# Kernel tuning notes

Hardware: AMD Instinct MI355X
Metric: run time of the kernel (lower is better)

## Reference

```python
import jax, jax.numpy as jnp
import numpy as np
import math

DIM = 512
HEADS = 8
DHEAD = DIM // HEADS            # 64
NB_FEATURES = int(DHEAD * math.log(DHEAD))  # 266
B, N = 2, 2048
CHUNK = 128                     # chunk size for the causal scan
EPS = 1e-4


def gaussian_orthogonal_random_matrix(nb_rows, nb_cols, rng):
    # blocks of orthogonal rows (Q^T of QR of a gaussian), scaled by chi-distributed norms
    blocks = []
    n_full = nb_rows // nb_cols
    for _ in range(n_full):
        q, _ = np.linalg.qr(rng.standard_normal((nb_cols, nb_cols)))
        blocks.append(q.T)
    rem = nb_rows - n_full * nb_cols
    if rem > 0:
        q, _ = np.linalg.qr(rng.standard_normal((nb_cols, nb_cols)))
        blocks.append(q.T[:rem])
    mat = np.concatenate(blocks, axis=0)
    multiplier = np.linalg.norm(rng.standard_normal((nb_rows, nb_cols)), axis=1)
    return (multiplier[:, None] * mat).astype(np.float32)


def setup_inputs() -> dict:
    key = jax.random.key(0)
    k1, k2, k3 = jax.random.split(key, 3)
    rng = np.random.default_rng(0)
    x = jax.random.normal(k1, (B, N, DIM), dtype=jnp.float32)
    w_qkv = jax.random.normal(k2, (DIM, 3 * DIM), dtype=jnp.float32) / math.sqrt(DIM)
    w_out = jax.random.normal(k3, (DIM, DIM), dtype=jnp.float32) / math.sqrt(DIM)
    b_out = jnp.zeros((DIM,), dtype=jnp.float32)
    proj = jnp.asarray(gaussian_orthogonal_random_matrix(NB_FEATURES, DHEAD, rng))
    return {"x": x, "w_qkv": w_qkv, "w_out": w_out, "b_out": b_out, "proj": proj}


def softmax_kernel(data, proj, is_query):
    # data: [b,h,n,d], proj: [m,d]
    d = data.shape[-1]
    data_normalizer = d ** -0.25
    ratio = proj.shape[0] ** -0.5
    data_dash = jnp.einsum('bhnd,md->bhnm', data_normalizer * data, proj)
    diag_data = jnp.sum(data * data, axis=-1, keepdims=True) * 0.5 * (data_normalizer ** 2)
    if is_query:
        stab = jnp.max(data_dash, axis=-1, keepdims=True)
    else:
        stab = jnp.max(data_dash)
    return ratio * (jnp.exp(data_dash - diag_data - stab) + EPS)


def causal_linear_attention(q, k, v, chunk=CHUNK):
    # q,k: [b,h,n,m]; v: [b,h,n,d]
    # out_n = sum_m q_nm * (sum_{i<=n} k_im v_i) / (sum_{i<=n} k_im)   (per-feature normalization,
    # identical to causal_linear_attention_noncuda), computed in chunks for memory efficiency.
    b, h, n, m = q.shape
    d = v.shape[-1]
    nc = n // chunk
    qc = jnp.moveaxis(q.reshape(b, h, nc, chunk, m), 2, 0)  # [nc,b,h,C,m]
    kc = jnp.moveaxis(k.reshape(b, h, nc, chunk, m), 2, 0)
    vc = jnp.moveaxis(v.reshape(b, h, nc, chunk, d), 2, 0)

    def step(carry, inp):
        kv_state, ksum_state = carry            # [b,h,m,d], [b,h,m]
        qch, kch, vch = inp                     # [b,h,C,m], [b,h,C,m], [b,h,C,d]
        ksum = ksum_state[:, :, None, :] + jnp.cumsum(kch, axis=2)          # [b,h,C,m]
        ctx = kv_state[:, :, None, :, :] + jnp.cumsum(
            jnp.einsum('bhcm,bhcd->bhcmd', kch, vch), axis=2)               # [b,h,C,m,d]
        out = jnp.einsum('bhcm,bhcmd->bhcd', qch, ctx / ksum[..., None])
        return (ctx[:, :, -1], ksum[:, :, -1]), out

    init = (jnp.zeros((b, h, m, d), q.dtype), jnp.zeros((b, h, m), q.dtype))
    _, outs = jax.lax.scan(step, init, (qc, kc, vc))
    return jnp.moveaxis(outs, 0, 2).reshape(b, h, n, d)


def reference(x, w_qkv, w_out, b_out, proj):
    b, n, _ = x.shape
    qkv = x @ w_qkv                                   # [b,n,3*dim]
    q, k, v = jnp.split(qkv, 3, axis=-1)
    split = lambda t: t.reshape(b, n, HEADS, DHEAD).transpose(0, 2, 1, 3)  # b h n d
    q, k, v = split(q), split(k), split(v)
    qp = softmax_kernel(q, proj, is_query=True)       # [b,h,n,m]
    kp = softmax_kernel(k, proj, is_query=False)
    out = causal_linear_attention(qp, kp, v)          # [b,h,n,d]
    out = out.transpose(0, 2, 1, 3).reshape(b, n, DIM)
    return out @ w_out + b_out
```

## Files before the change

### kernel.cpp

```cpp
#include <hip/hip_runtime.h>
#include <math.h>

#define DIMX 512
#define NHEADS 8
#define DH 64
#define MF 266
#define MP 272
#define NB 2
#define NSEQ 2048
#define NROWS (NB*NSEQ)
#define NBH 16
#define CHK 64
#define NCH 32
#define EPSF 1e-4f
#define LDT 40

typedef __attribute__((ext_vector_type(8))) short short8;
typedef __attribute__((ext_vector_type(4))) float f32x4;
typedef unsigned short ushort_t;

__device__ __forceinline__ unsigned fkey(float f){
    unsigned u = __float_as_uint(f);
    return (f < 0.0f) ? ~u : (u | 0x80000000u);
}
__device__ __forceinline__ float fdec(unsigned k){
    unsigned u = (k & 0x80000000u) ? (k & 0x7fffffffu) : ~k;
    return __uint_as_float(u);
}

__device__ __forceinline__ void bsplit(float a, ushort_t& h, ushort_t& l){
    unsigned u = __float_as_uint(a);
    unsigned r = (u + 0x7fffu + ((u >> 16) & 1u)) & 0xffff0000u;
    h = (ushort_t)(r >> 16);
    float res = a - __uint_as_float(r);
    unsigned v = __float_as_uint(res);
    unsigned r2 = v + 0x7fffu + ((v >> 16) & 1u);
    l = (ushort_t)(r2 >> 16);
}

__global__ __launch_bounds__(256) void split_kernel(
    const float* __restrict__ A, ushort_t* __restrict__ H, ushort_t* __restrict__ L, int total4)
{
    int i = blockIdx.x * 256 + threadIdx.x;
    if (i >= total4) return;
    float4 f = ((const float4*)A)[i];
    ushort_t h0,h1,h2,h3,l0,l1,l2,l3;
    bsplit(f.x,h0,l0); bsplit(f.y,h1,l1); bsplit(f.z,h2,l2); bsplit(f.w,h3,l3);
    ushort4 hv = make_ushort4(h0,h1,h2,h3), lv = make_ushort4(l0,l1,l2,l3);
    ((ushort4*)H)[i] = hv;
    ((ushort4*)L)[i] = lv;
}

__global__ __launch_bounds__(256) void splitT_kernel(
    const float* __restrict__ W, ushort_t* __restrict__ Th, ushort_t* __restrict__ Tl,
    int K, int N)
{
    __shared__ ushort_t Sh[64][72], Sl[64][72];
    const int k0 = blockIdx.y * 64, n0 = blockIdx.x * 64;
    const int tid = threadIdx.x;
    {
        const int kk = tid >> 4, nq = (tid & 15) * 4;
        for (int p = 0; p < 4; p++) {
            int k = p*16 + kk;
            float4 f = *(const float4*)&W[(size_t)(k0 + k)*N + n0 + nq];
            ushort_t h, l;
            bsplit(f.x,h,l); Sh[nq+0][k]=h; Sl[nq+0][k]=l;
            bsplit(f.y,h,l); Sh[nq+1][k]=h; Sl[nq+1][k]=l;
            bsplit(f.z,h,l); Sh[nq+2][k]=h; Sl[nq+2][k]=l;
            bsplit(f.w,h,l); Sh[nq+3][k]=h; Sl[nq+3][k]=l;
        }
    }
    __syncthreads();
    {
        const int n = tid >> 2, ks = (tid & 3) * 16;
        for (int q = 0; q < 2; q++) {
            uint4 vh = *(const uint4*)&Sh[n][ks + q*8];
            uint4 vl = *(const uint4*)&Sl[n][ks + q*8];
            *(uint4*)&Th[(size_t)(n0 + n)*K + k0 + ks + q*8] = vh;
            *(uint4*)&Tl[(size_t)(n0 + n)*K + k0 + ks + q*8] = vl;
        }
    }
}

__global__ __launch_bounds__(256) void gemm_bf16s(
    const ushort_t* __restrict__ Ah, const ushort_t* __restrict__ Al,
    const ushort_t* __restrict__ Bh, const ushort_t* __restrict__ Bl,
    const float* __restrict__ bias, float* __restrict__ C,
    int M, int N, int K)
{
    __shared__ ushort_t sAh[128*LDT], sAl[128*LDT], sBh[128*LDT], sBl[128*LDT];
    const int tid = threadIdx.x;
    const int m0 = blockIdx.y * 128, n0 = blockIdx.x * 128;
    const int lane = tid & 63, w = tid >> 6;
    const int wr = w >> 1, wc = w & 1;
    const int lr = lane & 15;
    const int lsu = (lane >> 4) * 8;
    const int r = tid >> 1, sg = (tid & 1) * 16;
    const size_t gA = (size_t)(m0 + r)*K + sg;
    const size_t gB = (size_t)(n0 + r)*K + sg;

    f32x4 acc[4][4];
    #pragma unroll
    for (int i=0;i<4;i++)
        #pragma unroll
        for (int j=0;j<4;j++) acc[i][j] = (f32x4){0.f,0.f,0.f,0.f};

    for (int k0 = 0; k0 < K; k0 += 32) {
        uint4 a0 = *(const uint4*)&Ah[gA + k0];
        uint4 a1 = *(const uint4*)&Ah[gA + k0 + 8];
        uint4 a2 = *(const uint4*)&Al[gA + k0];
        uint4 a3 = *(const uint4*)&Al[gA + k0 + 8];
        uint4 b0 = *(const uint4*)&Bh[gB + k0];
        uint4 b1 = *(const uint4*)&Bh[gB + k0 + 8];
        uint4 b2 = *(const uint4*)&Bl[gB + k0];
        uint4 b3 = *(const uint4*)&Bl[gB + k0 + 8];
        __syncthreads();
        *(uint4*)&sAh[r*LDT + sg]     = a0;
        *(uint4*)&sAh[r*LDT + sg + 8] = a1;
        *(uint4*)&sAl[r*LDT + sg]     = a2;
        *(uint4*)&sAl[r*LDT + sg + 8] = a3;
        *(uint4*)&sBh[r*LDT + sg]     = b0;
        *(uint4*)&sBh[r*LDT + sg + 8] = b1;
        *(uint4*)&sBl[r*LDT + sg]     = b2;
        *(uint4*)&sBl[r*LDT + sg + 8] = b3;
        __syncthreads();
        short8 afh[4], afl[4], bfh[4], bfl[4];
        #pragma unroll
        for (int f = 0; f < 4; f++) {
            int ra = (wr*64 + f*16 + lr)*LDT + lsu;
            int rb = (wc*64 + f*16 + lr)*LDT + lsu;
            afh[f] = *(const short8*)&sAh[ra];
            afl[f] = *(const short8*)&sAl[ra];
            bfh[f] = *(const short8*)&sBh[rb];
            bfl[f] = *(const short8*)&sBl[rb];
        }
        #pragma unroll
        for (int i = 0; i < 4; i++)
            #pragma unroll
            for (int j = 0; j < 4; j++) {
                acc[i][j] = __builtin_amdgcn_mfma_f32_16x16x32_bf16(afh[i], bfh[j], acc[i][j], 0, 0, 0);
                acc[i][j] = __builtin_amdgcn_mfma_f32_16x16x32_bf16(afh[i], bfl[j], acc[i][j], 0, 0, 0);
                acc[i][j] = __builtin_amdgcn_mfma_f32_16x16x32_bf16(afl[i], bfh[j], acc[i][j], 0, 0, 0);
            }
    }
    const int crow = (lane >> 4) * 4, ccol = lane & 15;
    #pragma unroll
    for (int i = 0; i < 4; i++) {
        #pragma unroll
        for (int j = 0; j < 4; j++) {
            int col = n0 + wc*64 + j*16 + ccol;
            float bb = bias ? bias[col] : 0.f;
            #pragma unroll
            for (int rr = 0; rr < 4; rr++) {
                int row = m0 + wr*64 + i*16 + crow + rr;
                C[(size_t)row*N + col] = acc[i][j][rr] + bb;
            }
        }
    }
}

template<bool IS_Q>
__global__ __launch_bounds__(256) void feat_kernel(
    const float* __restrict__ qkv, const float* __restrict__ proj,
    float* __restrict__ outp, float* __restrict__ diag_out,
    unsigned* __restrict__ gmax, int coff, float nrm, float ratio)
{
    __shared__ float As[64][68];
    __shared__ float Bs[16][MP+1];
    const int tid = threadIdx.x;
    const int tx = tid & 15, ty = tid >> 4;
    const int bh = blockIdx.y, b = bh >> 3, h = bh & 7;
    const int n0 = blockIdx.x * 64;
    {
        const int r = tid & 63, lq = tid >> 6;
        const float* src = &qkv[(size_t)(b*NSEQ + n0 + r)*(3*DIMX) + coff + h*DH];
        #pragma unroll
        for (int qq = 0; qq < 4; qq++) {
            int c = lq*16 + qq*4;
            float4 f = *(const float4*)&src[c];
            As[c+0][r]=f.x; As[c+1][r]=f.y; As[c+2][r]=f.z; As[c+3][r]=f.w;
        }
    }
    float dash[4][17];
    #pragma unroll
    for (int i=0;i<4;i++)
        #pragma unroll
        for (int j=0;j<17;j++) dash[i][j] = 0.f;
    float dsq[4] = {0.f,0.f,0.f,0.f};
    for (int s = 0; s < 4; s++) {
        __syncthreads();
        for (int idx = tid; idx < MP*4; idx += 256) {
            int m = idx >> 2, qq = idx & 3;
            float4 f = make_float4(0.f,0.f,0.f,0.f);
            if (m < MF) f = *(const float4*)&proj[m*DH + s*16 + qq*4];
            Bs[qq*4+0][m]=f.x; Bs[qq*4+1][m]=f.y; Bs[qq*4+2][m]=f.z; Bs[qq*4+3][m]=f.w;
        }
        __syncthreads();
        #pragma unroll
        for (int kk = 0; kk < 16; kk++) {
            float4 a = *(const float4*)&As[s*16+kk][ty*4];
            float ar[4] = {a.x,a.y,a.z,a.w};
            #pragma unroll
            for (int i=0;i<4;i++) dsq[i] = fmaf(ar[i], ar[i], dsq[i]);
            #pragma unroll
            for (int jj = 0; jj < 17; jj++) {
                float bv = Bs[kk][tx + 16*jj];
                #pragma unroll
                for (int i=0;i<4;i++) dash[i][jj] = fmaf(ar[i], bv, dash[i][jj]);
            }
        }
    }
    const size_t rbase = (size_t)bh*NSEQ + n0 + ty*4;
    if (IS_Q) {
        #pragma unroll
        for (int i=0;i<4;i++){
            float diag = 0.0625f * dsq[i];
            float mx = -1e30f;
            #pragma unroll
            for (int jj=0;jj<17;jj++){
                dash[i][jj] *= nrm;
                if (tx + 16*jj < MF) mx = fmaxf(mx, dash[i][jj]);
            }
            #pragma unroll
            for (int o=1;o<16;o<<=1) mx = fmaxf(mx, __shfl_xor(mx, o, 64));
            float* orow = &outp[(rbase + i)*MP];
            #pragma unroll
            for (int jj=0;jj<17;jj++){
                int m = tx + 16*jj;
                float v = (m < MF) ? ratio*(expf(dash[i][jj] - diag - mx) + EPSF) : 0.f;
                orow[m] = v;
            }
        }
    } else {
        float wmax = -1e30f;
        #pragma unroll
        for (int i=0;i<4;i++){
            float diag = 0.0625f * dsq[i];
            if (tx == 0) diag_out[rbase + i] = diag;
            float* orow = &outp[(rbase + i)*MP];
            #pragma unroll
            for (int jj=0;jj<17;jj++){
                float d = dash[i][jj] * nrm;
                int m = tx + 16*jj;
                orow[m] = d;
                if (m < MF) wmax = fmaxf(wmax, d);
            }
        }
        #pragma unroll
        for (int o=1;o<64;o<<=1) wmax = fmaxf(wmax, __shfl_xor(wmax, o, 64));
        if ((tid & 63) == 0) atomicMax(gmax, fkey(wmax));
    }
}

__global__ __launch_bounds__(256) void kexp_kernel(
    float* __restrict__ kp, const float* __restrict__ diagk,
    const unsigned* __restrict__ gmax, float ratio)
{
    unsigned idx4 = (blockIdx.x * 256u + threadIdx.x) * 4u;
    if (idx4 >= (unsigned)NBH*NSEQ*MP) return;
    const float stab = fdec(*gmax);
    int m = idx4 % MP;
    unsigned row = idx4 / MP;
    float dg = diagk[row];
    float4 v = *(float4*)&kp[idx4];
    float r[4] = {v.x,v.y,v.z,v.w};
    #pragma unroll
    for (int j = 0; j < 4; j++)
        r[j] = (m + j < MF) ? ratio * (expf(r[j] - dg - stab) + EPSF) : 0.f;
    *(float4*)&kp[idx4] = make_float4(r[0],r[1],r[2],r[3]);
}

__global__ __launch_bounds__(320) void chunk_sums_kernel(
    const float* __restrict__ kp, const float* __restrict__ qkv,
    float* __restrict__ ckv, float* __restrict__ cksum)
{
    __shared__ float vs[CHK][DH];
    const int tid = threadIdx.x;
    const int c = blockIdx.x, bh = blockIdx.y, b = bh >> 3, h = bh & 7;
    for (int idx = tid; idx < CHK*16; idx += 320) {
        int i = idx >> 4, q = idx & 15;
        *(float4*)&vs[i][q*4] =
            *(const float4*)&qkv[(size_t)(b*NSEQ + c*CHK + i)*(3*DIMX) + 2*DIMX + h*DH + q*4];
    }
    __syncthreads();
    if (tid >= 272) return;
    const int mg = tid % 68, dg = tid / 68;
    float acc[4][16] = {};
    float ks[4] = {0.f,0.f,0.f,0.f};
    const size_t kbase = (size_t)(bh*NSEQ + c*CHK)*MP + mg*4;
    for (int i = 0; i < CHK; i++) {
        float4 kv = *(const float4*)&kp[kbase + (size_t)i*MP];
        float kr[4] = {kv.x,kv.y,kv.z,kv.w};
        if (dg == 0) { ks[0]+=kr[0]; ks[1]+=kr[1]; ks[2]+=kr[2]; ks[3]+=kr[3]; }
        #pragma unroll
        for (int t = 0; t < 4; t++) {
            float4 vv = *(const float4*)&vs[i][dg*16 + t*4];
            float vr[4] = {vv.x,vv.y,vv.z,vv.w};
            #pragma unroll
            for (int mi=0;mi<4;mi++){
                acc[mi][t*4+0] = fmaf(kr[mi], vr[0], acc[mi][t*4+0]);
                acc[mi][t*4+1] = fmaf(kr[mi], vr[1], acc[mi][t*4+1]);
                acc[mi][t*4+2] = fmaf(kr[mi], vr[2], acc[mi][t*4+2]);
                acc[mi][t*4+3] = fmaf(kr[mi], vr[3], acc[mi][t*4+3]);
            }
        }
    }
    const size_t obase = ((size_t)(bh*NCH + c)*MP + mg*4)*DH + dg*16;
    #pragma unroll
    for (int mi=0;mi<4;mi++)
        #pragma unroll
        for (int t=0;t<4;t++)
            *(float4*)&ckv[obase + (size_t)mi*DH + t*4] =
                make_float4(acc[mi][t*4], acc[mi][t*4+1], acc[mi][t*4+2], acc[mi][t*4+3]);
    if (dg == 0) {
        #pragma unroll
        for (int mi=0;mi<4;mi++)
            cksum[(size_t)(bh*NCH + c)*MP + mg*4 + mi] = ks[mi];
    }
}

__global__ __launch_bounds__(256) void prefix_kv_kernel(float* __restrict__ ckv)
{
    const int bh = blockIdx.y;
    const int md = blockIdx.x * 256 + threadIdx.x;
    float run = 0.f;
    #pragma unroll
    for (int c = 0; c < NCH; c++) {
        size_t idx = (size_t)(bh*NCH + c)*MP*DH + md;
        float v = ckv[idx];
        ckv[idx] = run;
        run += v;
    }
}

__global__ __launch_bounds__(320) void prefix_ksum_kernel(float* __restrict__ cksum)
{
    const int bh = blockIdx.x;
    const int m = threadIdx.x;
    if (m >= MP) return;
    float run = 0.f;
    #pragma unroll
    for (int c = 0; c < NCH; c++) {
        size_t idx = (size_t)(bh*NCH + c)*MP + m;
        float v = cksum[idx];
        cksum[idx] = run;
        run += v;
    }
}

__global__ __launch_bounds__(320) void qprime_kernel(
    float* __restrict__ qp, const float* __restrict__ kp, const float* __restrict__ cksum)
{
    const int c = blockIdx.x, bh = blockIdx.y;
    const int m = threadIdx.x;
    if (m >= MP) return;
    float run = cksum[(size_t)(bh*NCH + c)*MP + m];
    size_t base = (size_t)(bh*NSEQ + c*CHK)*MP + m;
    for (int i = 0; i < CHK; i++) {
        size_t idx = base + (size_t)i*MP;
        run += kp[idx];
        float q = qp[idx];
        qp[idx] = (m < MF) ? q / run : 0.f;
    }
}

__global__ __launch_bounds__(256) void attn_kernel(
    const float* __restrict__ qp, const float* __restrict__ kp,
    const float* __restrict__ qkv, const float* __restrict__ ckv,
    ushort_t* __restrict__ aout_h, ushort_t* __restrict__ aout_l)
{
    __shared__ float Qs[16][68];
    __shared__ float Ks[16][68];
    __shared__ float Ss[16][68];
    __shared__ float Vs[CHK][68];
    __shared__ float P[CHK][76];
    const int tid = threadIdx.x, tx = tid & 15, ty = tid >> 4;
    const int c = blockIdx.x, bh = blockIdx.y, b = bh >> 3, hh = bh & 7;
    const size_t rowg = (size_t)bh*NSEQ + c*CHK;
    const size_t rowx = (size_t)b*NSEQ + c*CHK;

    for (int idx = tid; idx < CHK*16; idx += 256) {
        int i = idx >> 4, q = idx & 15;
        *(float4*)&Vs[i][q*4] =
            *(const float4*)&qkv[(rowx + i)*(3*DIMX) + 2*DIMX + hh*DH + q*4];
    }

    float accP[4][4] = {};
    float accO[4][4] = {};
    const int ldi = tid >> 2, ldq = tid & 3;
    const int smm = tid >> 4, smq = tid & 15;
    for (int m0 = 0; m0 < MP; m0 += 16) {
        __syncthreads();
        {
            float4 f = *(const float4*)&qp[(rowg + ldi)*MP + m0 + ldq*4];
            Qs[ldq*4+0][ldi]=f.x; Qs[ldq*4+1][ldi]=f.y; Qs[ldq*4+2][ldi]=f.z; Qs[ldq*4+3][ldi]=f.w;
            float4 g = *(const float4*)&kp[(rowg + ldi)*MP + m0 + ldq*4];
            Ks[ldq*4+0][ldi]=g.x; Ks[ldq*4+1][ldi]=g.y; Ks[ldq*4+2][ldi]=g.z; Ks[ldq*4+3][ldi]=g.w;
            *(float4*)&Ss[smm][smq*4] =
                *(const float4*)&ckv[((size_t)(bh*NCH + c)*MP + m0 + smm)*DH + smq*4];
        }
        __syncthreads();
        #pragma unroll
        for (int kk = 0; kk < 16; kk++) {
            float4 a = *(const float4*)&Qs[kk][ty*4];
            float4 bk = *(const float4*)&Ks[kk][tx*4];
            float4 bs = *(const float4*)&Ss[kk][tx*4];
            float ar[4] = {a.x,a.y,a.z,a.w};
            float kr[4] = {bk.x,bk.y,bk.z,bk.w};
            float sr[4] = {bs.x,bs.y,bs.z,bs.w};
            #pragma unroll
            for (int i=0;i<4;i++)
                #pragma unroll
                for (int j=0;j<4;j++) {
                    accP[i][j] = fmaf(ar[i], kr[j], accP[i][j]);
                    accO[i][j] = fmaf(ar[i], sr[j], accO[i][j]);
                }
        }
    }
    #pragma unroll
    for (int i=0;i<4;i++){
        int r = ty*4+i;
        float4 o;
        o.x = (tx*4+0 <= r) ? accP[i][0] : 0.f;
        o.y = (tx*4+1 <= r) ? accP[i][1] : 0.f;
        o.z = (tx*4+2 <= r) ? accP[i][2] : 0.f;
        o.w = (tx*4+3 <= r) ? accP[i][3] : 0.f;
        *(float4*)&P[r][tx*4] = o;
    }
    __syncthreads();
    #pragma unroll 4
    for (int kk = 0; kk < CHK; kk++) {
        float4 vv = *(const float4*)&Vs[kk][tx*4];
        float vr[4] = {vv.x,vv.y,vv.z,vv.w};
        #pragma unroll
        for (int i=0;i<4;i++){
            float a = P[ty*4+i][kk];
            accO[i][0] = fmaf(a, vr[0], accO[i][0]);
            accO[i][1] = fmaf(a, vr[1], accO[i][1]);
            accO[i][2] = fmaf(a, vr[2], accO[i][2]);
            accO[i][3] = fmaf(a, vr[3], accO[i][3]);
        }
    }
    #pragma unroll
    for (int i=0;i<4;i++){
        ushort_t h0,h1,h2,h3,l0,l1,l2,l3;
        bsplit(accO[i][0],h0,l0); bsplit(accO[i][1],h1,l1);
        bsplit(accO[i][2],h2,l2); bsplit(accO[i][3],h3,l3);
        size_t o = (rowx + ty*4 + i)*DIMX + hh*DH + tx*4;
        *(ushort4*)&aout_h[o] = make_ushort4(h0,h1,h2,h3);
        *(ushort4*)&aout_l[o] = make_ushort4(l0,l1,l2,l3);
    }
}

extern "C" void kernel_launch(void* const* d_in, const int* in_sizes, int n_in,
                              void* d_out, int out_size, void* d_ws, size_t ws_size,
                              hipStream_t stream)
{
    (void)in_sizes; (void)n_in; (void)out_size; (void)ws_size;
    const float* x     = (const float*)d_in[0];
    const float* w_qkv = (const float*)d_in[1];
    const float* w_out = (const float*)d_in[2];
    const float* b_out = (const float*)d_in[3];
    const float* proj  = (const float*)d_in[4];
    float* out = (float*)d_out;

    char* ws = (char*)d_ws;
    size_t off = 0;
    auto alloc = [&](size_t bytes) -> char* {
        char* p = ws + off;
        off += (bytes + 255) & ~(size_t)255;
        return p;
    };
    float* qkv       = (float*)alloc((size_t)NROWS*3*DIMX*sizeof(float));
    float* qp        = (float*)alloc((size_t)NBH*NSEQ*MP*sizeof(float));
    float* kp        = (float*)alloc((size_t)NBH*NSEQ*MP*sizeof(float));
    float* diagk     = (float*)alloc((size_t)NBH*NSEQ*sizeof(float));
    unsigned* gmax   = (unsigned*)alloc(256);
    float* ckv       = (float*)alloc((size_t)NBH*NCH*MP*DH*sizeof(float));
    float* cksum     = (float*)alloc((size_t)NBH*NCH*MP*sizeof(float));
    ushort_t* xs_h   = (ushort_t*)alloc((size_t)NROWS*DIMX*sizeof(ushort_t));
    ushort_t* xs_l   = (ushort_t*)alloc((size_t)NROWS*DIMX*sizeof(ushort_t));
    ushort_t* wqt_h  = (ushort_t*)alloc((size_t)(3*DIMX)*DIMX*sizeof(ushort_t));
    ushort_t* wqt_l  = (ushort_t*)alloc((size_t)(3*DIMX)*DIMX*sizeof(ushort_t));
    ushort_t* wot_h  = (ushort_t*)alloc((size_t)DIMX*DIMX*sizeof(ushort_t));
    ushort_t* wot_l  = (ushort_t*)alloc((size_t)DIMX*DIMX*sizeof(ushort_t));
    ushort_t* aout_h = xs_h;
    ushort_t* aout_l = xs_l;

    const float nrm   = (float)pow(64.0, -0.25);
    const float ratio = (float)(1.0 / sqrt(266.0));

    hipMemsetAsync(gmax, 0, sizeof(unsigned), stream);
    split_kernel<<<dim3((NROWS*DIMX/4 + 255)/256), 256, 0, stream>>>(x, xs_h, xs_l, NROWS*DIMX/4);
    splitT_kernel<<<dim3(3*DIMX/64, DIMX/64), 256, 0, stream>>>(w_qkv, wqt_h, wqt_l, DIMX, 3*DIMX);
    splitT_kernel<<<dim3(DIMX/64, DIMX/64), 256, 0, stream>>>(w_out, wot_h, wot_l, DIMX, DIMX);
    gemm_bf16s<<<dim3(3*DIMX/128, NROWS/128), 256, 0, stream>>>(
        xs_h, xs_l, wqt_h, wqt_l, nullptr, qkv, NROWS, 3*DIMX, DIMX);
    feat_kernel<true ><<<dim3(32, 16), 256, 0, stream>>>(qkv, proj, qp, nullptr, nullptr, 0, nrm, ratio);
    feat_kernel<false><<<dim3(32, 16), 256, 0, stream>>>(qkv, proj, kp, diagk, gmax, DIMX, nrm, ratio);
    kexp_kernel<<<dim3((NBH*NSEQ*MP)/1024), 256, 0, stream>>>(kp, diagk, gmax, ratio);
    chunk_sums_kernel<<<dim3(NCH, NBH), 320, 0, stream>>>(kp, qkv, ckv, cksum);
    prefix_kv_kernel<<<dim3(68, NBH), 256, 0, stream>>>(ckv);
    prefix_ksum_kernel<<<dim3(NBH), 320, 0, stream>>>(cksum);
    qprime_kernel<<<dim3(NCH, NBH), 320, 0, stream>>>(qp, kp, cksum);
    attn_kernel<<<dim3(NCH, NBH), 256, 0, stream>>>(qp, kp, qkv, ckv, aout_h, aout_l);
    gemm_bf16s<<<dim3(DIMX/128, NROWS/128), 256, 0, stream>>>(
        aout_h, aout_l, wot_h, wot_l, b_out, out, NROWS, DIMX, DIMX);
}
```

Before: 295.0 us.

## Run attention chunk kernel on bf16x3 MFMA with split feature buffers

The intra-chunk attention kernel moves from scalar FP32 FMAs to MFMA bf16 instructions, using a three-product hi/lo split to keep close to FP32 accuracy. To feed it, the query/key features and the prefix KV state are stored as hi/lo bf16 pairs, padded to 288 features and transposed to d-major. Chunk sums and the prefix scan now produce that transposed split layout. The cost is extra split/reconstruct arithmetic in several kernels and some precision loss from the three-product bf16 emulation.

New measurement: 268.8 us. 1.1x faster.

```diff
diff --git a/kernel.cpp b/kernel.cpp
--- a/kernel.cpp
+++ b/kernel.cpp
@@ -6,6 +6,7 @@
 #define DH 64
 #define MF 266
 #define MP 272
+#define MPS 288
 #define NB 2
 #define NSEQ 2048
 #define NROWS (NB*NSEQ)
@@ -14,6 +15,7 @@
 #define NCH 32
 #define EPSF 1e-4f
 #define LDT 40
+#define LDP 72
 
 typedef __attribute__((ext_vector_type(8))) short short8;
 typedef __attribute__((ext_vector_type(4))) float f32x4;
@@ -26,6 +28,9 @@
 __device__ __forceinline__ float fdec(unsigned k){
     unsigned u = (k & 0x80000000u) ? (k & 0x7fffffffu) : ~k;
     return __uint_as_float(u);
+}
+__device__ __forceinline__ float b2f(ushort_t u){
+    return __uint_as_float(((unsigned)u) << 16);
 }
 
 __device__ __forceinline__ void bsplit(float a, ushort_t& h, ushort_t& l){
@@ -46,9 +51,8 @@
     float4 f = ((const float4*)A)[i];
     ushort_t h0,h1,h2,h3,l0,l1,l2,l3;
     bsplit(f.x,h0,l0); bsplit(f.y,h1,l1); bsplit(f.z,h2,l2); bsplit(f.w,h3,l3);
-    ushort4 hv = make_ushort4(h0,h1,h2,h3), lv = make_ushort4(l0,l1,l2,l3);
-    ((ushort4*)H)[i] = hv;
-    ((ushort4*)L)[i] = lv;
+    ((ushort4*)H)[i] = make_ushort4(h0,h1,h2,h3);
+    ((ushort4*)L)[i] = make_ushort4(l0,l1,l2,l3);
 }
 
 __global__ __launch_bounds__(256) void splitT_kernel(
@@ -162,8 +166,9 @@
 template<bool IS_Q>
 __global__ __launch_bounds__(256) void feat_kernel(
     const float* __restrict__ qkv, const float* __restrict__ proj,
-    float* __restrict__ outp, float* __restrict__ diag_out,
-    unsigned* __restrict__ gmax, int coff, float nrm, float ratio)
+    float* __restrict__ dashout, ushort_t* __restrict__ oh, ushort_t* __restrict__ ol,
+    float* __restrict__ diag_out, unsigned* __restrict__ gmax,
+    int coff, float nrm, float ratio)
 {
     __shared__ float As[64][68];
     __shared__ float Bs[16][MP+1];
@@ -223,12 +228,15 @@
             }
             #pragma unroll
             for (int o=1;o<16;o<<=1) mx = fmaxf(mx, __shfl_xor(mx, o, 64));
-            float* orow = &outp[(rbase + i)*MP];
+            ushort_t* orh = &oh[(rbase + i)*MPS];
+            ushort_t* orl = &ol[(rbase + i)*MPS];
             #pragma unroll
             for (int jj=0;jj<17;jj++){
                 int m = tx + 16*jj;
                 float v = (m < MF) ? ratio*(expf(dash[i][jj] - diag - mx) + EPSF) : 0.f;
-                orow[m] = v;
+                ushort_t hh2, ll2;
+                bsplit(v, hh2, ll2);
+                orh[m] = hh2; orl[m] = ll2;
             }
         }
     } else {
@@ -237,7 +245,7 @@
         for (int i=0;i<4;i++){
             float diag = 0.0625f * dsq[i];
             if (tx == 0) diag_out[rbase + i] = diag;
-            float* orow = &outp[(rbase + i)*MP];
+            float* orow = &dashout[(rbase + i)*MP];
             #pragma unroll
             for (int jj=0;jj<17;jj++){
                 float d = dash[i][jj] * nrm;
@@ -253,26 +261,37 @@
 }
 
 __global__ __launch_bounds__(256) void kexp_kernel(
-    float* __restrict__ kp, const float* __restrict__ diagk,
-    const unsigned* __restrict__ gmax, float ratio)
-{
-    unsigned idx4 = (blockIdx.x * 256u + threadIdx.x) * 4u;
-    if (idx4 >= (unsigned)NBH*NSEQ*MP) return;
-    const float stab = fdec(*gmax);
-    int m = idx4 % MP;
-    unsigned row = idx4 / MP;
-    float dg = diagk[row];
-    float4 v = *(float4*)&kp[idx4];
-    float r[4] = {v.x,v.y,v.z,v.w};
-    #pragma unroll
-    for (int j = 0; j < 4; j++)
-        r[j] = (m + j < MF) ? ratio * (expf(r[j] - dg - stab) + EPSF) : 0.f;
-    *(float4*)&kp[idx4] = make_float4(r[0],r[1],r[2],r[3]);
+    const float* __restrict__ dash, const float* __restrict__ diagk,
+    const unsigned* __restrict__ gmax,
+    ushort_t* __restrict__ kph, ushort_t* __restrict__ kpl, float ratio)
+{
+    unsigned gid = blockIdx.x * 256u + threadIdx.x;
+    if (gid >= (unsigned)NBH*NSEQ*(MPS/4)) return;
+    unsigned row = gid / (MPS/4);
+    int mq = (int)(gid % (MPS/4)) * 4;
+    ushort4 h4 = make_ushort4(0,0,0,0), l4 = make_ushort4(0,0,0,0);
+    if (mq < MP) {
+        const float stab = fdec(*gmax);
+        float dg = diagk[row];
+        float4 v = *(const float4*)&dash[(size_t)row*MP + mq];
+        float r[4] = {v.x,v.y,v.z,v.w};
+        ushort_t hh[4], ll[4];
+        #pragma unroll
+        for (int j = 0; j < 4; j++) {
+            float kv = (mq + j < MF) ? ratio * (expf(r[j] - dg - stab) + EPSF) : 0.f;
+            bsplit(kv, hh[j], ll[j]);
+        }
+        h4 = make_ushort4(hh[0],hh[1],hh[2],hh[3]);
+        l4 = make_ushort4(ll[0],ll[1],ll[2],ll[3]);
+    }
+    *(ushort4*)&kph[(size_t)row*MPS + mq] = h4;
+    *(ushort4*)&kpl[(size_t)row*MPS + mq] = l4;
 }
 
 __global__ __launch_bounds__(320) void chunk_sums_kernel(
-    const float* __restrict__ kp, const float* __restrict__ qkv,
-    float* __restrict__ ckv, float* __restrict__ cksum)
+    const ushort_t* __restrict__ kph, const ushort_t* __restrict__ kpl,
+    const float* __restrict__ qkv,
+    float* __restrict__ ckvT, float* __restrict__ cksum)
 {
     __shared__ float vs[CHK][DH];
     const int tid = threadIdx.x;
@@ -287,10 +306,12 @@
     const int mg = tid % 68, dg = tid / 68;
     float acc[4][16] = {};
     float ks[4] = {0.f,0.f,0.f,0.f};
-    const size_t kbase = (size_t)(bh*NSEQ + c*CHK)*MP + mg*4;
+    const size_t kbase = (size_t)(bh*NSEQ + c*CHK)*MPS + mg*4;
     for (int i = 0; i < CHK; i++) {
-        float4 kv = *(const float4*)&kp[kbase + (size_t)i*MP];
-        float kr[4] = {kv.x,kv.y,kv.z,kv.w};
+        ushort4 kh = *(const ushort4*)&kph[kbase + (size_t)i*MPS];
+        ushort4 kl = *(const ushort4*)&kpl[kbase + (size_t)i*MPS];
+        float kr[4] = {b2f(kh.x)+b2f(kl.x), b2f(kh.y)+b2f(kl.y),
+                       b2f(kh.z)+b2f(kl.z), b2f(kh.w)+b2f(kl.w)};
         if (dg == 0) { ks[0]+=kr[0]; ks[1]+=kr[1]; ks[2]+=kr[2]; ks[3]+=kr[3]; }
         #pragma unroll
         for (int t = 0; t < 4; t++) {
@@ -305,13 +326,13 @@
             }
         }
     }
-    const size_t obase = ((size_t)(bh*NCH + c)*MP + mg*4)*DH + dg*16;
+    const size_t tbase = (size_t)(bh*NCH + c)*64;
     #pragma unroll
-    for (int mi=0;mi<4;mi++)
-        #pragma unroll
-        for (int t=0;t<4;t++)
-            *(float4*)&ckv[obase + (size_t)mi*DH + t*4] =
-                make_float4(acc[mi][t*4], acc[mi][t*4+1], acc[mi][t*4+2], acc[mi][t*4+3]);
+    for (int dd = 0; dd < 16; dd++) {
+        int d = dg*16 + dd;
+        *(float4*)&ckvT[(tbase + d)*MP + mg*4] =
+            make_float4(acc[0][dd], acc[1][dd], acc[2][dd], acc[3][dd]);
+    }
     if (dg == 0) {
         #pragma unroll
         for (int mi=0;mi<4;mi++)
@@ -319,17 +340,29 @@
     }
 }
 
-__global__ __launch_bounds__(256) void prefix_kv_kernel(float* __restrict__ ckv)
+__global__ __launch_bounds__(256) void prefix_ckvT_kernel(
+    const float* __restrict__ ckvT, ushort_t* __restrict__ cth, ushort_t* __restrict__ ctl)
 {
     const int bh = blockIdx.y;
-    const int md = blockIdx.x * 256 + threadIdx.x;
-    float run = 0.f;
-    #pragma unroll
-    for (int c = 0; c < NCH; c++) {
-        size_t idx = (size_t)(bh*NCH + c)*MP*DH + md;
-        float v = ckv[idx];
-        ckv[idx] = run;
-        run += v;
+    const int dm = blockIdx.x * 256 + threadIdx.x;
+    if (dm >= 64*MPS) return;
+    const int d = dm / MPS, m = dm % MPS;
+    if (m < MP) {
+        float run = 0.f;
+        #pragma unroll
+        for (int c = 0; c < NCH; c++) {
+            size_t row = (size_t)(bh*NCH + c)*64 + d;
+            ushort_t h, l;
+            bsplit(run, h, l);
+            cth[row*MPS + m] = h; ctl[row*MPS + m] = l;
+            run += ckvT[row*MP + m];
+        }
+    } else {
+        #pragma unroll
+        for (int c = 0; c < NCH; c++) {
+            size_t row = (size_t)(bh*NCH + c)*64 + d;
+            cth[row*MPS + m] = 0; ctl[row*MPS + m] = 0;
+        }
     }
 }
 
@@ -349,106 +382,177 @@
 }
 
 __global__ __launch_bounds__(320) void qprime_kernel(
-    float* __restrict__ qp, const float* __restrict__ kp, const float* __restrict__ cksum)
+    ushort_t* __restrict__ qph, ushort_t* __restrict__ qpl,
+    const ushort_t* __restrict__ kph, const ushort_t* __restrict__ kpl,
+    const float* __restrict__ cksum)
 {
     const int c = blockIdx.x, bh = blockIdx.y;
     const int m = threadIdx.x;
-    if (m >= MP) return;
-    float run = cksum[(size_t)(bh*NCH + c)*MP + m];
-    size_t base = (size_t)(bh*NSEQ + c*CHK)*MP + m;
-    for (int i = 0; i < CHK; i++) {
-        size_t idx = base + (size_t)i*MP;
-        run += kp[idx];
-        float q = qp[idx];
-        qp[idx] = (m < MF) ? q / run : 0.f;
-    }
-}
-
-__global__ __launch_bounds__(256) void attn_kernel(
-    const float* __restrict__ qp, const float* __restrict__ kp,
-    const float* __restrict__ qkv, const float* __restrict__ ckv,
+    if (m >= MPS) return;
+    size_t base = (size_t)(bh*NSEQ + c*CHK)*MPS + m;
+    if (m < MF) {
+        float run = cksum[(size_t)(bh*NCH + c)*MP + m];
+        for (int i = 0; i < CHK; i++) {
+            size_t idx = base + (size_t)i*MPS;
+            run += b2f(kph[idx]) + b2f(kpl[idx]);
+            float q = b2f(qph[idx]) + b2f(qpl[idx]);
+            q /= run;
+            ushort_t h, l;
+            bsplit(q, h, l);
+            qph[idx] = h; qpl[idx] = l;
+        }
+    } else {
+        for (int i = 0; i < CHK; i++) {
+            size_t idx = base + (size_t)i*MPS;
+            qph[idx] = 0; qpl[idx] = 0;
+        }
+    }
+}
+
+__global__ __launch_bounds__(256) void attn_mfma(
+    const ushort_t* __restrict__ qph, const ushort_t* __restrict__ qpl,
+    const ushort_t* __restrict__ kph, const ushort_t* __restrict__ kpl,
+    const ushort_t* __restrict__ cth, const ushort_t* __restrict__ ctl,
+    const float* __restrict__ qkv,
     ushort_t* __restrict__ aout_h, ushort_t* __restrict__ aout_l)
 {
-    __shared__ float Qs[16][68];
-    __shared__ float Ks[16][68];
-    __shared__ float Ss[16][68];
-    __shared__ float Vs[CHK][68];
-    __shared__ float P[CHK][76];
-    const int tid = threadIdx.x, tx = tid & 15, ty = tid >> 4;
+    __shared__ ushort_t tQh[64*LDT], tQl[64*LDT];
+    __shared__ ushort_t tKh[64*LDT], tKl[64*LDT];
+    __shared__ ushort_t tSh[64*LDT], tSl[64*LDT];
+    __shared__ ushort_t VTh[64*LDP], VTl[64*LDP];
+    __shared__ ushort_t Ph[64*LDP],  Pl[64*LDP];
+    const int tid = threadIdx.x;
     const int c = blockIdx.x, bh = blockIdx.y, b = bh >> 3, hh = bh & 7;
     const size_t rowg = (size_t)bh*NSEQ + c*CHK;
     const size_t rowx = (size_t)b*NSEQ + c*CHK;
-
-    for (int idx = tid; idx < CHK*16; idx += 256) {
-        int i = idx >> 4, q = idx & 15;
-        *(float4*)&Vs[i][q*4] =
-            *(const float4*)&qkv[(rowx + i)*(3*DIMX) + 2*DIMX + hh*DH + q*4];
-    }
-
-    float accP[4][4] = {};
-    float accO[4][4] = {};
-    const int ldi = tid >> 2, ldq = tid & 3;
-    const int smm = tid >> 4, smq = tid & 15;
-    for (int m0 = 0; m0 < MP; m0 += 16) {
+    const size_t sbase = (size_t)(bh*NCH + c)*64;
+
+    {
+        const int j = tid >> 2, dq = (tid & 3) * 16;
+        const float* vsrc = &qkv[(rowx + j)*(3*DIMX) + 2*DIMX + hh*DH + dq];
+        #pragma unroll
+        for (int p = 0; p < 4; p++) {
+            float4 f = *(const float4*)&vsrc[p*4];
+            float vr[4] = {f.x,f.y,f.z,f.w};
+            #pragma unroll
+            for (int wv = 0; wv < 4; wv++) {
+                ushort_t h, l;
+                bsplit(vr[wv], h, l);
+                VTh[(dq + p*4 + wv)*LDP + j] = h;
+                VTl[(dq + p*4 + wv)*LDP + j] = l;
+            }
+        }
+    }
+
+    const int lane = tid & 63, w = tid >> 6;
+    const int wr = w >> 1, wc = w & 1;
+    const int fr = lane & 15, fk = (lane >> 4) * 8;
+    const int srow = tid >> 2, sseg = (tid & 3) * 8;
+    f32x4 accP[2][2], accO[2][2];
+    #pragma unroll
+    for (int i=0;i<2;i++)
+        #pragma unroll
+        for (int j=0;j<2;j++){ accP[i][j]=(f32x4){0,0,0,0}; accO[i][j]=(f32x4){0,0,0,0}; }
+
+    for (int m0 = 0; m0 < MPS; m0 += 32) {
+        uint4 gq_h = *(const uint4*)&qph[(rowg + srow)*MPS + m0 + sseg];
+        uint4 gq_l = *(const uint4*)&qpl[(rowg + srow)*MPS + m0 + sseg];
+        uint4 gk_h = *(const uint4*)&kph[(rowg + srow)*MPS + m0 + sseg];
+        uint4 gk_l = *(const uint4*)&kpl[(rowg + srow)*MPS + m0 + sseg];
+        uint4 gs_h = *(const uint4*)&cth[(sbase + srow)*MPS + m0 + sseg];
+        uint4 gs_l = *(const uint4*)&ctl[(sbase + srow)*MPS + m0 + sseg];
         __syncthreads();
-        {
-            float4 f = *(const float4*)&qp[(rowg + ldi)*MP + m0 + ldq*4];
-            Qs[ldq*4+0][ldi]=f.x; Qs[ldq*4+1][ldi]=f.y; Qs[ldq*4+2][ldi]=f.z; Qs[ldq*4+3][ldi]=f.w;
-            float4 g = *(const float4*)&kp[(rowg + ldi)*MP + m0 + ldq*4];
-            Ks[ldq*4+0][ldi]=g.x; Ks[ldq*4+1][ldi]=g.y; Ks[ldq*4+2][ldi]=g.z; Ks[ldq*4+3][ldi]=g.w;
-            *(float4*)&Ss[smm][smq*4] =
-                *(const float4*)&ckv[((size_t)(bh*NCH + c)*MP + m0 + smm)*DH + smq*4];
-        }
+        *(uint4*)&tQh[srow*LDT + sseg] = gq_h;
+        *(uint4*)&tQl[srow*LDT + sseg] = gq_l;
+        *(uint4*)&tKh[srow*LDT + sseg] = gk_h;
+        *(uint4*)&tKl[srow*LDT + sseg] = gk_l;
+        *(uint4*)&tSh[srow*LDT + sseg] = gs_h;
+        *(uint4*)&tSl[srow*LDT + sseg] = gs_l;
         __syncthreads();
-        #pragma unroll
-        for (int kk = 0; kk < 16; kk++) {
-            float4 a = *(const float4*)&Qs[kk][ty*4];
-            float4 bk = *(const float4*)&Ks[kk][tx*4];
-            float4 bs = *(const float4*)&Ss[kk][tx*4];
-            float ar[4] = {a.x,a.y,a.z,a.w};
-            float kr[4] = {bk.x,bk.y,bk.z,bk.w};
-            float sr[4] = {bs.x,bs.y,bs.z,bs.w};
-            #pragma unroll
-            for (int i=0;i<4;i++)
+        short8 aQh[2], aQl[2], bKh[2], bKl[2], bSh[2], bSl[2];
+        #pragma unroll
+        for (int f = 0; f < 2; f++) {
+            int ra = (wr*32 + f*16 + fr)*LDT + fk;
+            int rb = (wc*32 + f*16 + fr)*LDT + fk;
+            aQh[f] = *(const short8*)&tQh[ra];
+            aQl[f] = *(const short8*)&tQl[ra];
+            bKh[f] = *(const short8*)&tKh[rb];
+            bKl[f] = *(const short8*)&tKl[rb];
+            bSh[f] = *(const short8*)&tSh[rb];
+            bSl[f] = *(const short8*)&tSl[rb];
+        }
+        #pragma unroll
+        for (int i = 0; i < 2; i++)
+            #pragma unroll
+            for (int j = 0; j < 2; j++) {
+                accP[i][j] = __builtin_amdgcn_mfma_f32_16x16x32_bf16(aQh[i], bKh[j], accP[i][j], 0, 0, 0);
+                accP[i][j] = __builtin_amdgcn_mfma_f32_16x16x32_bf16(aQh[i], bKl[j], accP[i][j], 0, 0, 0);
+                accP[i][j] = __builtin_amdgcn_mfma_f32_16x16x32_bf16(aQl[i], bKh[j], accP[i][j], 0, 0, 0);
+                accO[i][j] = __builtin_amdgcn_mfma_f32_16x16x32_bf16(aQh[i], bSh[j], accO[i][j], 0, 0, 0);
+                accO[i][j] = __builtin_amdgcn_mfma_f32_16x16x32_bf16(aQh[i], bSl[j], accO[i][j], 0, 0, 0);
+                accO[i][j] = __builtin_amdgcn_mfma_f32_16x16x32_bf16(aQl[i], bSh[j], accO[i][j], 0, 0, 0);
+            }
+    }
+
+    __syncthreads();
+    {
+        const int crow = (lane >> 4) * 4, ccol = lane & 15;
+        #pragma unroll
+        for (int i = 0; i < 2; i++)
+            #pragma unroll
+            for (int j = 0; j < 2; j++) {
+                int colg = wc*32 + j*16 + ccol;
                 #pragma unroll
-                for (int j=0;j<4;j++) {
-                    accP[i][j] = fmaf(ar[i], kr[j], accP[i][j]);
-                    accO[i][j] = fmaf(ar[i], sr[j], accO[i][j]);
+                for (int rr = 0; rr < 4; rr++) {
+                    int rowg2 = wr*32 + i*16 + crow + rr;
+                    float v = (colg <= rowg2) ? accP[i][j][rr] : 0.f;
+                    ushort_t h, l;
+                    bsplit(v, h, l);
+                    Ph[rowg2*LDP + colg] = h;
+                    Pl[rowg2*LDP + colg] = l;
                 }
-        }
-    }
+            }
+    }
+    __syncthreads();
+
     #pragma unroll
-    for (int i=0;i<4;i++){
-        int r = ty*4+i;
-        float4 o;
-        o.x = (tx*4+0 <= r) ? accP[i][0] : 0.f;
-        o.y = (tx*4+1 <= r) ? accP[i][1] : 0.f;
-        o.z = (tx*4+2 <= r) ? accP[i][2] : 0.f;
-        o.w = (tx*4+3 <= r) ? accP[i][3] : 0.f;
-        *(float4*)&P[r][tx*4] = o;
-    }
-    __syncthreads();
-    #pragma unroll 4
-    for (int kk = 0; kk < CHK; kk++) {
-        float4 vv = *(const float4*)&Vs[kk][tx*4];
-        float vr[4] = {vv.x,vv.y,vv.z,vv.w};
-        #pragma unroll
-        for (int i=0;i<4;i++){
-            float a = P[ty*4+i][kk];
-            accO[i][0] = fmaf(a, vr[0], accO[i][0]);
-            accO[i][1] = fmaf(a, vr[1], accO[i][1]);
-            accO[i][2] = fmaf(a, vr[2], accO[i][2]);
-            accO[i][3] = fmaf(a, vr[3], accO[i][3]);
-        }
-    }
-    #pragma unroll
-    for (int i=0;i<4;i++){
-        ushort_t h0,h1,h2,h3,l0,l1,l2,l3;
-        bsplit(accO[i][0],h0,l0); bsplit(accO[i][1],h1,l1);
-        bsplit(accO[i][2],h2,l2); bsplit(accO[i][3],h3,l3);
-        size_t o = (rowx + ty*4 + i)*DIMX + hh*DH + tx*4;
-        *(ushort4*)&aout_h[o] = make_ushort4(h0,h1,h2,h3);
-        *(ushort4*)&aout_l[o] = make_ushort4(l0,l1,l2,l3);
+    for (int js = 0; js < 2; js++) {
+        short8 aPh[2], aPl[2], bVh[2], bVl[2];
+        #pragma unroll
+        for (int f = 0; f < 2; f++) {
+            int ra = (wr*32 + f*16 + fr)*LDP + js*32 + fk;
+            int rb = (wc*32 + f*16 + fr)*LDP + js*32 + fk;
+            aPh[f] = *(const short8*)&Ph[ra];
+            aPl[f] = *(const short8*)&Pl[ra];
+            bVh[f] = *(const short8*)&VTh[rb];
+            bVl[f] = *(const short8*)&VTl[rb];
+        }
+        #pragma unroll
+        for (int i = 0; i < 2; i++)
+            #pragma unroll
+            for (int j = 0; j < 2; j++) {
+                accO[i][j] = __builtin_amdgcn_mfma_f32_16x16x32_bf16(aPh[i], bVh[j], accO[i][j], 0, 0, 0);
+                accO[i][j] = __builtin_amdgcn_mfma_f32_16x16x32_bf16(aPh[i], bVl[j], accO[i][j], 0, 0, 0);
+                accO[i][j] = __builtin_amdgcn_mfma_f32_16x16x32_bf16(aPl[i], bVh[j], accO[i][j], 0, 0, 0);
+            }
+    }
+
+    {
+        const int crow = (lane >> 4) * 4, ccol = lane & 15;
+        #pragma unroll
+        for (int i = 0; i < 2; i++)
+            #pragma unroll
+            for (int j = 0; j < 2; j++) {
+                int d = wc*32 + j*16 + ccol;
+                #pragma unroll
+                for (int rr = 0; rr < 4; rr++) {
+                    int row = wr*32 + i*16 + crow + rr;
+                    size_t o = (rowx + row)*DIMX + hh*DH + d;
+                    ushort_t h, l;
+                    bsplit(accO[i][j][rr], h, l);
+                    aout_h[o] = h; aout_l[o] = l;
+                }
+            }
     }
 }
 
@@ -472,18 +576,23 @@
         return p;
     };
     float* qkv       = (float*)alloc((size_t)NROWS*3*DIMX*sizeof(float));
-    float* qp        = (float*)alloc((size_t)NBH*NSEQ*MP*sizeof(float));
-    float* kp        = (float*)alloc((size_t)NBH*NSEQ*MP*sizeof(float));
+    float* dash      = (float*)alloc((size_t)NBH*NSEQ*MP*sizeof(float));
+    ushort_t* qph    = (ushort_t*)alloc((size_t)NBH*NSEQ*MPS*sizeof(ushort_t));
+    ushort_t* qpl    = (ushort_t*)alloc((size_t)NBH*NSEQ*MPS*sizeof(ushort_t));
+    ushort_t* kph    = (ushort_t*)alloc((size_t)NBH*NSEQ*MPS*sizeof(ushort_t));
+    ushort_t* kpl    = (ushort_t*)alloc((size_t)NBH*NSEQ*MPS*sizeof(ushort_t));
+    ushort_t* cth    = (ushort_t*)alloc((size_t)NBH*NCH*64*MPS*sizeof(ushort_t));
+    ushort_t* ctl    = (ushort_t*)alloc((size_t)NBH*NCH*64*MPS*sizeof(ushort_t));
+    float* cksum     = (float*)alloc((size_t)NBH*NCH*MP*sizeof(float));
     float* diagk     = (float*)alloc((size_t)NBH*NSEQ*sizeof(float));
     unsigned* gmax   = (unsigned*)alloc(256);
-    float* ckv       = (float*)alloc((size_t)NBH*NCH*MP*DH*sizeof(float));
-    float* cksum     = (float*)alloc((size_t)NBH*NCH*MP*sizeof(float));
     ushort_t* xs_h   = (ushort_t*)alloc((size_t)NROWS*DIMX*sizeof(ushort_t));
     ushort_t* xs_l   = (ushort_t*)alloc((size_t)NROWS*DIMX*sizeof(ushort_t));
     ushort_t* wqt_h  = (ushort_t*)alloc((size_t)(3*DIMX)*DIMX*sizeof(ushort_t));
     ushort_t* wqt_l  = (ushort_t*)alloc((size_t)(3*DIMX)*DIMX*sizeof(ushort_t));
     ushort_t* wot_h  = (ushort_t*)alloc((size_t)DIMX*DIMX*sizeof(ushort_t));
     ushort_t* wot_l  = (ushort_t*)alloc((size_t)DIMX*DIMX*sizeof(ushort_t));
+    float* ckvT      = dash;
     ushort_t* aout_h = xs_h;
     ushort_t* aout_l = xs_l;
 
@@ -496,14 +605,18 @@
     splitT_kernel<<<dim3(DIMX/64, DIMX/64), 256, 0, stream>>>(w_out, wot_h, wot_l, DIMX, DIMX);
     gemm_bf16s<<<dim3(3*DIMX/128, NROWS/128), 256, 0, stream>>>(
         xs_h, xs_l, wqt_h, wqt_l, nullptr, qkv, NROWS, 3*DIMX, DIMX);
-    feat_kernel<true ><<<dim3(32, 16), 256, 0, stream>>>(qkv, proj, qp, nullptr, nullptr, 0, nrm, ratio);
-    feat_kernel<false><<<dim3(32, 16), 256, 0, stream>>>(qkv, proj, kp, diagk, gmax, DIMX, nrm, ratio);
-    kexp_kernel<<<dim3((NBH*NSEQ*MP)/1024), 256, 0, stream>>>(kp, diagk, gmax, ratio);
-    chunk_sums_kernel<<<dim3(NCH, NBH), 320, 0, stream>>>(kp, qkv, ckv, cksum);
-    prefix_kv_kernel<<<dim3(68, NBH), 256, 0, stream>>>(ckv);
+    feat_kernel<true ><<<dim3(32, 16), 256, 0, stream>>>(
+        qkv, proj, nullptr, qph, qpl, nullptr, nullptr, 0, nrm, ratio);
+    feat_kernel<false><<<dim3(32, 16), 256, 0, stream>>>(
+        qkv, proj, dash, nullptr, nullptr, diagk, gmax, DIMX, nrm, ratio);
+    kexp_kernel<<<dim3((NBH*NSEQ*(MPS/4) + 255)/256), 256, 0, stream>>>(
+        dash, diagk, gmax, kph, kpl, ratio);
+    chunk_sums_kernel<<<dim3(NCH, NBH), 320, 0, stream>>>(kph, kpl, qkv, ckvT, cksum);
+    prefix_ckvT_kernel<<<dim3((64*MPS + 255)/256, NBH), 256, 0, stream>>>(ckvT, cth, ctl);
     prefix_ksum_kernel<<<dim3(NBH), 320, 0, stream>>>(cksum);
-    qprime_kernel<<<dim3(NCH, NBH), 320, 0, stream>>>(qp, kp, cksum);
-    attn_kernel<<<dim3(NCH, NBH), 256, 0, stream>>>(qp, kp, qkv, ckv, aout_h, aout_l);
+    qprime_kernel<<<dim3(NCH, NBH), 320, 0, stream>>>(qph, qpl, kph, kpl, cksum);
+    attn_mfma<<<dim3(NCH, NBH), 256, 0, stream>>>(
+        qph, qpl, kph, kpl, cth, ctl, qkv, aout_h, aout_l);
     gemm_bf16s<<<dim3(DIMX/128, NROWS/128), 256, 0, stream>>>(
         aout_h, aout_l, wot_h, wot_l, b_out, out, NROWS, DIMX, DIMX);
 }
```
